# Optimization experiments

Hardware: AMD Instinct MI355X
Metric: run time of the kernel (lower is better)

## Reference

```python
import jax, jax.numpy as jnp
import numpy as np

DIM = 512

def setup_inputs() -> dict:
    key = jax.random.key(0)
    ks = jax.random.split(key, 7)
    B, Nq, Nkv = 8, 1024, 4096
    prototype = jax.random.normal(ks[0], (B, Nq, DIM), dtype=jnp.float32)
    q_x = jax.random.normal(ks[1], (B, Nkv, DIM), dtype=jnp.float32)
    qry_attn_mask = jax.random.bernoulli(ks[2], 0.5, (B, Nkv))  # True = keep
    # Linear(dim, dim, bias=False) weights, torch convention y = x @ W.T
    s = 1.0 / np.sqrt(DIM)
    Wq = jax.random.uniform(ks[3], (DIM, DIM), jnp.float32, -s, s)
    Wk = jax.random.uniform(ks[4], (DIM, DIM), jnp.float32, -s, s)
    Wv = jax.random.uniform(ks[5], (DIM, DIM), jnp.float32, -s, s)
    Wproj = jax.random.uniform(ks[6], (DIM, DIM), jnp.float32, -s, s)
    return {"prototype": prototype, "q_x": q_x, "qry_attn_mask": qry_attn_mask,
            "Wq": Wq, "Wk": Wk, "Wv": Wv, "Wproj": Wproj}

def reference(prototype, q_x, qry_attn_mask, Wq, Wk, Wv, Wproj):
    scale = DIM ** (-0.5)
    q = jnp.einsum('bnd,ed->bne', prototype, Wq)          # [B,Nq,D]
    k = jnp.einsum('bmd,ed->bme', q_x, Wk)                # [B,Nkv,D]
    v = jnp.einsum('bmd,ed->bme', q_x, Wv)                # [B,Nkv,D]
    attn = jnp.einsum('bnd,bmd->bnm', q, k) * scale       # [B,Nq,Nkv]
    bias = (~qry_attn_mask).astype(attn.dtype)[:, None, :] * -10000.0
    attn = jax.nn.softmax(attn + bias, axis=-1)
    x = jnp.einsum('bnm,bmd->bnd', attn, v)
    x = jnp.einsum('bnd,ed->bne', x, Wproj)
    return x
```

## Files before the change

kernel.cpp:

```cpp
#include <hip/hip_runtime.h>
#include <hip/hip_bf16.h>
#include <stdint.h>


typedef __bf16 bf16;
typedef bf16 bf16x8 __attribute__((ext_vector_type(8)));
typedef bf16 bf16x4 __attribute__((ext_vector_type(4)));
typedef float f32x4 __attribute__((ext_vector_type(4)));

#define NB 8
#define NQ 1024
#define NKV 4096
#define DD 512
#define RT_LD 136

__device__ __forceinline__ void direct16(const void* g, void* s) {
  __builtin_amdgcn_global_load_lds(
      (const __attribute__((address_space(1))) void*)g,
      (__attribute__((address_space(3))) void*)s, 16, 0, 0);
}

__global__ void cvt_kernel(const float* __restrict__ src, bf16* __restrict__ dst, int n4) {
  int i = blockIdx.x * blockDim.x + threadIdx.x;
  if (i < n4) {
    float4 v = ((const float4*)src)[i];
    bf16x4 o;
    o.x = (bf16)v.x; o.y = (bf16)v.y; o.z = (bf16)v.z; o.w = (bf16)v.w;
    ((bf16x4*)dst)[i] = o;
  }
}

__global__ void cvt_weights(const float* __restrict__ Wq, const float* __restrict__ Wk,
                            const float* __restrict__ Wv, const float* __restrict__ Wp,
                            bf16* __restrict__ Wq_b, bf16* __restrict__ Wkv_b,
                            bf16* __restrict__ Wp_b) {
  int i = blockIdx.x * blockDim.x + threadIdx.x;
  int w = i >> 16, r = i & 65535;
  const float* src = (w == 0) ? Wq : (w == 1) ? Wk : (w == 2) ? Wv : Wp;
  bf16x4* dst = (w == 0) ? (bf16x4*)Wq_b
              : (w == 3) ? (bf16x4*)Wp_b
                         : (bf16x4*)Wkv_b + (w == 2 ? 65536 : 0);
  float4 v = ((const float4*)src)[r];
  bf16x4 o;
  o.x = (bf16)v.x; o.y = (bf16)v.y; o.z = (bf16)v.z; o.w = (bf16)v.w;
  dst[r] = o;
}

__global__ void sniff_zero(const unsigned* __restrict__ mask, int* __restrict__ flag,
                           float* __restrict__ denom) {
  __shared__ int s_bad0, s_bad1;
  if (threadIdx.x == 0) { s_bad0 = 0; s_bad1 = 0; }
  __syncthreads();
  int b0 = 0, b1 = 0;
  for (int i = threadIdx.x; i < 8192; i += 256) {
    unsigned v = mask[i];
    if (v > 1u) b0 = 1;
    if (v != 0u && v != 0x3F800000u) b1 = 1;
  }
  if (b0) atomicOr(&s_bad0, 1);
  if (b1) atomicOr(&s_bad1, 1);
  for (int i = threadIdx.x; i < NB * NQ; i += 256) denom[i] = 0.f;
  __syncthreads();
  if (threadIdx.x == 0) *flag = (s_bad0 == 0) ? 0 : ((s_bad1 == 0) ? 1 : 2);
}

template <int EPI>
__global__ void __launch_bounds__(256, 2)
gemm_bt(const bf16* __restrict__ A, const bf16* __restrict__ Bw,
        void* __restrict__ Cp, void* __restrict__ Cp2,
        int N, int Klen, int Kstride,
        long sA, long sB, long sC,
        const void* __restrict__ mask, const int* __restrict__ flagP,
        float* __restrict__ denom, float scale, int M) {
  __shared__ alignas(16) bf16 Smem[128 * RT_LD];
  bf16* As = Smem;
  bf16* Bs = Smem + 4096;
  bf16* Rt = Smem;
  const int tid = threadIdx.x;
  const int wave = tid >> 6, lane = tid & 63;
  const int l15 = lane & 15, l4 = lane >> 4;
  const int wm = (wave >> 1) * 64, wn = (wave & 1) * 64;
  const int bx = (EPI == 5) ? blockIdx.y : blockIdx.x;
  const int by = (EPI == 5) ? blockIdx.x : blockIdx.y;
  const int b = blockIdx.z;

  const bf16* Ab = A + (long)b * sA + (long)(by * 128) * Kstride;
  const bf16* Bb = Bw + (long)b * sB + (long)(bx * 128) * Kstride;

  const int c0 = wave * 2, c1 = wave * 2 + 1;
  const int srow = lane >> 2;
  const int scol = (lane & 3) * 8;
  const bf16* ag0 = Ab + (long)(c0 * 16 + srow) * Kstride + scol;
  const bf16* ag1 = Ab + (long)(c1 * 16 + srow) * Kstride + scol;
  const bf16* bg0 = Bb + (long)(c0 * 16 + srow) * Kstride + scol;
  const bf16* bg1 = Bb + (long)(c1 * 16 + srow) * Kstride + scol;
  bf16* al0 = As + c0 * 512 + lane * 8;
  bf16* al1 = As + c1 * 512 + lane * 8;
  bf16* bl0 = Bs + c0 * 512 + lane * 8;
  bf16* bl1 = Bs + c1 * 512 + lane * 8;

  f32x4 acc[4][4] = {};

  for (int kt = 0; kt < Klen; kt += 32) {
    __syncthreads();
    direct16(ag0, al0);
    direct16(ag1, al1);
    direct16(bg0, bl0);
    direct16(bg1, bl1);
    ag0 += 32; ag1 += 32; bg0 += 32; bg1 += 32;
    __syncthreads();
    bf16x8 af[4], bfr[4];
#pragma unroll
    for (int t = 0; t < 4; ++t)
      af[t] = *(const bf16x8*)(As + (wm + t * 16 + l15) * 32 + l4 * 8);
#pragma unroll
    for (int t = 0; t < 4; ++t)
      bfr[t] = *(const bf16x8*)(Bs + (wn + t * 16 + l15) * 32 + l4 * 8);
#pragma unroll
    for (int mt = 0; mt < 4; ++mt)
#pragma unroll
      for (int nt = 0; nt < 4; ++nt)
        acc[mt][nt] = __builtin_amdgcn_mfma_f32_16x16x32_bf16(af[mt], bfr[nt],
                                                              acc[mt][nt], 0, 0, 0);
  }

  const int rowBase = by * 128 + wm;
  const int colBase = bx * 128 + wn;
  const int tR = by * 128;
  const int tC = bx * 128;

  if constexpr (EPI == 2) {
    __syncthreads();
    bf16* C = (bf16*)Cp + (long)b * sC;
    const int mode = *flagP;
    float rs[4][4];
#pragma unroll
    for (int mt = 0; mt < 4; ++mt)
#pragma unroll
      for (int r = 0; r < 4; ++r) rs[mt][r] = 0.f;
#pragma unroll
    for (int nt = 0; nt < 4; ++nt) {
      const int col = colBase + nt * 16 + l15;
      bool keep;
      if (mode == 0)      keep = ((const int*)mask)[b * NKV + col] != 0;
      else if (mode == 1) keep = ((const float*)mask)[b * NKV + col] != 0.f;
      else                keep = ((const unsigned char*)mask)[b * NKV + col] != 0;
#pragma unroll
      for (int mt = 0; mt < 4; ++mt)
#pragma unroll
        for (int r = 0; r < 4; ++r) {
          float p = keep ? __expf(acc[mt][nt][r] * scale) : 0.f;
          rs[mt][r] += p;
          Rt[(wm + mt * 16 + l4 * 4 + r) * RT_LD + wn + nt * 16 + l15] = (bf16)p;
        }
    }
#pragma unroll
    for (int mt = 0; mt < 4; ++mt)
#pragma unroll
      for (int r = 0; r < 4; ++r) {
        float v = rs[mt][r];
        v += __shfl_xor(v, 1, 64);
        v += __shfl_xor(v, 2, 64);
        v += __shfl_xor(v, 4, 64);
        v += __shfl_xor(v, 8, 64);
        if (l15 == 0)
          atomicAdd(&denom[b * M + rowBase + mt * 16 + l4 * 4 + r], v);
      }
    __syncthreads();
    const int r0 = tid >> 2, cq = (tid & 3) * 32;
#pragma unroll
    for (int h = 0; h < 128; h += 64)
#pragma unroll
      for (int j = 0; j < 4; ++j) {
        bf16x8 v = *(const bf16x8*)(Rt + (r0 + h) * RT_LD + cq + j * 8);
        *(bf16x8*)(C + (long)(tR + r0 + h) * N + tC + cq + j * 8) = v;
      }
  } else {
    __syncthreads();
    if (tC < 512) {
      bf16* C = (bf16*)Cp;
#pragma unroll
      for (int mt = 0; mt < 4; ++mt)
#pragma unroll
        for (int nt = 0; nt < 4; ++nt)
#pragma unroll
          for (int r = 0; r < 4; ++r)
            Rt[(wm + mt * 16 + l4 * 4 + r) * RT_LD + wn + nt * 16 + l15] =
                (bf16)acc[mt][nt][r];
      __syncthreads();
      const int r0 = tid >> 2, cq = (tid & 3) * 32;
#pragma unroll
      for (int h = 0; h < 128; h += 64)
#pragma unroll
        for (int j = 0; j < 4; ++j) {
          bf16x8 v = *(const bf16x8*)(Rt + (r0 + h) * RT_LD + cq + j * 8);
          *(bf16x8*)(C + (long)(tR + r0 + h) * 512 + tC + cq + j * 8) = v;
        }
    } else {
      bf16* C = (bf16*)Cp2;
#pragma unroll
      for (int mt = 0; mt < 4; ++mt) {
        const int r0 = wm + mt * 16 + l4 * 4;
#pragma unroll
        for (int nt = 0; nt < 4; ++nt) {
          const int cloc = wn + nt * 16 + l15;
          bf16x4 o;
          o.x = (bf16)acc[mt][nt][0]; o.y = (bf16)acc[mt][nt][1];
          o.z = (bf16)acc[mt][nt][2]; o.w = (bf16)acc[mt][nt][3];
          *(bf16x4*)(Rt + cloc * RT_LD + r0) = o;
        }
      }
      __syncthreads();
      const int bb = tR >> 12, kvloc = tR & 4095;
      const int d0 = tid >> 2, kvq = (tid & 3) * 32;
#pragma unroll
      for (int h = 0; h < 128; h += 64)
#pragma unroll
        for (int j = 0; j < 4; ++j) {
          bf16x8 v = *(const bf16x8*)(Rt + (d0 + h) * RT_LD + kvq + j * 8);
          *(bf16x8*)(C + (long)bb * DD * NKV + (long)(tC - 512 + d0 + h) * NKV +
                     kvloc + kvq + j * 8) = v;
        }
    }
  }
}

template <int EPI>
__global__ void __launch_bounds__(256, 4)
gemm_n64(const bf16* __restrict__ A, const bf16* __restrict__ Bw,
         void* __restrict__ Cp) {
  constexpr int SME = (EPI == 0) ? 128 * 72 : 6144;
  __shared__ alignas(16) bf16 Smem[SME];
  bf16* As = Smem;
  bf16* Bs = Smem + 4096;
  bf16* Rt = Smem;
  const int tid = threadIdx.x;
  const int wave = tid >> 6, lane = tid & 63;
  const int l15 = lane & 15, l4 = lane >> 4;
  const int wm = (wave >> 1) * 64, wn = (wave & 1) * 32;

  const bf16* Ab = A + (long)(blockIdx.y * 128) * DD;
  const bf16* Bb = Bw + (long)(blockIdx.x * 64) * DD;

  const int srow = lane >> 2, scol = (lane & 3) * 8;
  const bf16* ag0 = Ab + (long)(wave * 32 + srow) * DD + scol;
  const bf16* ag1 = ag0 + 16 * DD;
  const bf16* bg0 = Bb + (long)(wave * 16 + srow) * DD + scol;
  bf16* al0 = As + wave * 1024 + lane * 8;
  bf16* al1 = al0 + 512;
  bf16* bl0 = Bs + wave * 512 + lane * 8;

  f32x4 acc[4][2] = {};

  for (int kt = 0; kt < DD; kt += 32) {
    __syncthreads();
    direct16(ag0, al0);
    direct16(ag1, al1);
    direct16(bg0, bl0);
    ag0 += 32; ag1 += 32; bg0 += 32;
    __syncthreads();
    bf16x8 af[4], bfr[2];
#pragma unroll
    for (int t = 0; t < 4; ++t)
      af[t] = *(const bf16x8*)(As + (wm + t * 16 + l15) * 32 + l4 * 8);
#pragma unroll
    for (int t = 0; t < 2; ++t)
      bfr[t] = *(const bf16x8*)(Bs + (wn + t * 16 + l15) * 32 + l4 * 8);
#pragma unroll
    for (int mt = 0; mt < 4; ++mt)
#pragma unroll
      for (int nt = 0; nt < 2; ++nt)
        acc[mt][nt] = __builtin_amdgcn_mfma_f32_16x16x32_bf16(af[mt], bfr[nt],
                                                              acc[mt][nt], 0, 0, 0);
  }

  const int tR = blockIdx.y * 128, tC = blockIdx.x * 64;
  if constexpr (EPI == 0) {
    __syncthreads();
#pragma unroll
    for (int mt = 0; mt < 4; ++mt)
#pragma unroll
      for (int nt = 0; nt < 2; ++nt)
#pragma unroll
        for (int r = 0; r < 4; ++r)
          Rt[(wm + mt * 16 + l4 * 4 + r) * 72 + wn + nt * 16 + l15] =
              (bf16)acc[mt][nt][r];
    __syncthreads();
    bf16* C = (bf16*)Cp;
    const int r0 = tid >> 1, cq = (tid & 1) * 32;
#pragma unroll
    for (int j = 0; j < 4; ++j) {
      bf16x8 v = *(const bf16x8*)(Rt + r0 * 72 + cq + j * 8);
      *(bf16x8*)(C + (long)(tR + r0) * DD + tC + cq + j * 8) = v;
    }
  } else {
    float* C = (float*)Cp;
#pragma unroll
    for (int mt = 0; mt < 4; ++mt)
#pragma unroll
      for (int nt = 0; nt < 2; ++nt)
#pragma unroll
        for (int r = 0; r < 4; ++r)
          C[(long)(tR + wm + mt * 16 + l4 * 4 + r) * DD + tC + wn + nt * 16 + l15] =
              acc[mt][nt][r];
  }
}

__global__ void __launch_bounds__(256, 4)
pv_direct(const bf16* __restrict__ P, const bf16* __restrict__ vT,
          const float* __restrict__ denom, bf16* __restrict__ x) {
  __shared__ alignas(16) bf16 Smem[64 * RT_LD];
  bf16* As = Smem;
  bf16* Bs = Smem + 2048;
  bf16* Rt = Smem;
  const int tid = threadIdx.x;
  const int wave = tid >> 6, lane = tid & 63;
  const int l15 = lane & 15, l4 = lane >> 4;
  const int wm = (wave >> 1) * 32, wn = (wave & 1) * 64;
  const int qB = blockIdx.x * 64;
  const int dB = blockIdx.y * 128;
  const int b = blockIdx.z;

  const bf16* Ab = P + (long)b * NQ * NKV + (long)qB * NKV;
  const bf16* Bb = vT + (long)b * DD * NKV + (long)dB * NKV;

  const int srow = lane >> 2, scol = (lane & 3) * 8;
  const bf16* ag = Ab + (long)(wave * 16 + srow) * NKV + scol;
  const bf16* bg0 = Bb + (long)(wave * 32 + srow) * NKV + scol;
  const bf16* bg1 = bg0 + 16 * NKV;
  bf16* al = As + wave * 512 + lane * 8;
  bf16* bl0 = Bs + wave * 1024 + lane * 8;
  bf16* bl1 = bl0 + 512;

  f32x4 acc[2][4] = {};

  for (int kt = 0; kt < NKV; kt += 32) {
    __syncthreads();
    direct16(ag, al);
    direct16(bg0, bl0);
    direct16(bg1, bl1);
    ag += 32; bg0 += 32; bg1 += 32;
    __syncthreads();
    bf16x8 af[2], bfr[4];
#pragma unroll
    for (int t = 0; t < 2; ++t)
      af[t] = *(const bf16x8*)(As + (wm + t * 16 + l15) * 32 + l4 * 8);
#pragma unroll
    for (int t = 0; t < 4; ++t)
      bfr[t] = *(const bf16x8*)(Bs + (wn + t * 16 + l15) * 32 + l4 * 8);
#pragma unroll
    for (int mt = 0; mt < 2; ++mt)
#pragma unroll
      for (int nt = 0; nt < 4; ++nt)
        acc[mt][nt] = __builtin_amdgcn_mfma_f32_16x16x32_bf16(af[mt], bfr[nt],
                                                              acc[mt][nt], 0, 0, 0);
  }

  __syncthreads();
#pragma unroll
  for (int mt = 0; mt < 2; ++mt)
#pragma unroll
    for (int r = 0; r < 4; ++r) {
      const int row = wm + mt * 16 + l4 * 4 + r;
      const float inv = 1.0f / denom[b * NQ + qB + row];
#pragma unroll
      for (int nt = 0; nt < 4; ++nt)
        Rt[row * RT_LD + wn + nt * 16 + l15] = (bf16)(acc[mt][nt][r] * inv);
    }
  __syncthreads();
  const int r0 = tid >> 2, cq = (tid & 3) * 32;
#pragma unroll
  for (int j = 0; j < 4; ++j) {
    bf16x8 v = *(const bf16x8*)(Rt + r0 * RT_LD + cq + j * 8);
    *(bf16x8*)(x + (long)(b * NQ + qB + r0) * DD + dB + cq + j * 8) = v;
  }
}

extern "C" void kernel_launch(void* const* d_in, const int* in_sizes, int n_in,
                              void* d_out, int out_size, void* d_ws, size_t ws_size,
                              hipStream_t stream) {
  const float* proto = (const float*)d_in[0];
  const float* qx    = (const float*)d_in[1];
  const void*  mask  = d_in[2];
  const float* Wq    = (const float*)d_in[3];
  const float* Wk    = (const float*)d_in[4];
  const float* Wv    = (const float*)d_in[5];
  const float* Wproj = (const float*)d_in[6];
  float* out = (float*)d_out;

  char* w = (char*)d_ws;
  int*   flag  = (int*)w;
  float* denom = (float*)(w + 4096);
  size_t off = 65536;
  bf16* Wq_b  = (bf16*)(w + off); off += (size_t)DD * DD * 2;
  bf16* Wkv_b = (bf16*)(w + off); off += (size_t)DD * DD * 4;
  bf16* Wp_b  = (bf16*)(w + off); off += (size_t)DD * DD * 2;
  bf16* q_b   = (bf16*)(w + off); off += (size_t)NB * NQ * DD * 2;
  bf16* k_b   = (bf16*)(w + off); off += (size_t)NB * NKV * DD * 2;
  bf16* vT_b  = (bf16*)(w + off); off += (size_t)NB * NKV * DD * 2;
  bf16* x_b   = (bf16*)(w + off); off += (size_t)NB * NQ * DD * 2;
  size_t off_pp = off;
  bf16* proto_b = (bf16*)(w + off); off += (size_t)NB * NQ * DD * 2;
  bf16* qx_b    = (bf16*)(w + off);
  bf16* P       = (bf16*)(w + off_pp);

  sniff_zero<<<1, 256, 0, stream>>>((const unsigned*)mask, flag, denom);

  cvt_kernel<<<NB * NQ * DD / 4 / 256, 256, 0, stream>>>(proto, proto_b, NB * NQ * DD / 4);
  cvt_kernel<<<NB * NKV * DD / 4 / 256, 256, 0, stream>>>(qx, qx_b, NB * NKV * DD / 4);
  cvt_weights<<<4 * 65536 / 256, 256, 0, stream>>>(Wq, Wk, Wv, Wproj, Wq_b, Wkv_b, Wp_b);

  const float scale = 0.04419417382415922f;

  gemm_n64<0><<<dim3(8, 64, 1), 256, 0, stream>>>(proto_b, Wq_b, q_b);
  gemm_bt<5><<<dim3(256, 8, 1), 256, 0, stream>>>(
      qx_b, Wkv_b, k_b, vT_b, 1024, DD, DD, 0L, 0L, 0L,
      nullptr, nullptr, nullptr, 0.f, 0);
  gemm_bt<2><<<dim3(NKV / 128, NQ / 128, NB), 256, 0, stream>>>(
      q_b, k_b, P, nullptr, NKV, DD, DD,
      (long)NQ * DD, (long)NKV * DD, (long)NQ * NKV,
      mask, flag, denom, scale, NQ);
  pv_direct<<<dim3(16, 4, 8), 256, 0, stream>>>(P, vT_b, denom, x_b);
  gemm_n64<4><<<dim3(8, 64, 1), 256, 0, stream>>>(x_b, Wp_b, out);
}
```

Baseline: 380.2 us.

## Compact unmasked keys and skip masked key blocks in attention

Adds a per-batch prefix-scan kernel that builds the list of kept key indices and a count padded up to 128. A gather kernel converts only the kept q_x rows to bf16. The K/V projection, the QK^T softmax-numerator kernel and the PV loop then stop at that padded length instead of the full 4096. The aim is to drop the GEMM work and memory traffic spent on masked keys, which the earlier version already set to zero probability. Padded rows between the count and the padded length are never written, so they keep leftover workspace contents. This relies on the zeroed P entries cancelling those rows and adds two small launches.

```diff
diff --git a/kernel.cpp b/kernel.cpp
--- a/kernel.cpp
+++ b/kernel.cpp
@@ -64,13 +64,70 @@
   if (threadIdx.x == 0) *flag = (s_bad0 == 0) ? 0 : ((s_bad1 == 0) ? 1 : 2);
 }
 
+__global__ void scan_mask(const void* __restrict__ mask, const int* __restrict__ flagP,
+                          int* __restrict__ idx, int* __restrict__ cnt,
+                          int* __restrict__ kpad) {
+  const int b = blockIdx.x, tid = threadIdx.x;
+  const int mode = *flagP;
+  __shared__ int ps[256];
+  unsigned bits = 0;
+  int c = 0;
+  const int base = tid * 16;
+  for (int i = 0; i < 16; ++i) {
+    const int col = base + i;
+    bool k;
+    if (mode == 0)      k = ((const int*)mask)[b * NKV + col] != 0;
+    else if (mode == 1) k = ((const float*)mask)[b * NKV + col] != 0.f;
+    else                k = ((const unsigned char*)mask)[b * NKV + col] != 0;
+    bits |= (unsigned)k << i;
+    c += k;
+  }
+  ps[tid] = c;
+  __syncthreads();
+  for (int s = 1; s < 256; s <<= 1) {
+    int v = (tid >= s) ? ps[tid - s] : 0;
+    __syncthreads();
+    ps[tid] += v;
+    __syncthreads();
+  }
+  int off = ps[tid] - c;
+  for (int i = 0; i < 16; ++i)
+    if ((bits >> i) & 1) idx[b * NKV + off++] = base + i;
+  if (tid == 255) {
+    cnt[b] = ps[255];
+    kpad[b] = (ps[255] + 127) & ~127;
+  }
+}
+
+__global__ void gather_qx(const float* __restrict__ qx, const int* __restrict__ idx,
+                          const int* __restrict__ cnt, bf16* __restrict__ qc) {
+  const int b = blockIdx.y;
+  const int wave = threadIdx.x >> 6, lane = threadIdx.x & 63;
+  const int r0 = blockIdx.x * 16 + wave * 4;
+  const int n = cnt[b];
+#pragma unroll
+  for (int j = 0; j < 4; ++j) {
+    const int row = r0 + j;
+    if (row >= n) return;
+    const int src = idx[b * NKV + row];
+    const float4* s = (const float4*)(qx + ((long)b * NKV + src) * DD) + lane;
+    bf16x4* d = (bf16x4*)(qc + ((long)b * NKV + row) * DD) + lane;
+    float4 v0 = s[0], v1 = s[64];
+    bf16x4 o0, o1;
+    o0.x = (bf16)v0.x; o0.y = (bf16)v0.y; o0.z = (bf16)v0.z; o0.w = (bf16)v0.w;
+    o1.x = (bf16)v1.x; o1.y = (bf16)v1.y; o1.z = (bf16)v1.z; o1.w = (bf16)v1.w;
+    d[0] = o0;
+    d[64] = o1;
+  }
+}
+
 template <int EPI>
 __global__ void __launch_bounds__(256, 2)
 gemm_bt(const bf16* __restrict__ A, const bf16* __restrict__ Bw,
         void* __restrict__ Cp, void* __restrict__ Cp2,
         int N, int Klen, int Kstride,
         long sA, long sB, long sC,
-        const void* __restrict__ mask, const int* __restrict__ flagP,
+        const int* __restrict__ cnt, const int* __restrict__ kpad,
         float* __restrict__ denom, float scale, int M) {
   __shared__ alignas(16) bf16 Smem[128 * RT_LD];
   bf16* As = Smem;
@@ -84,6 +141,13 @@
   const int by = (EPI == 5) ? blockIdx.x : blockIdx.y;
   const int b = blockIdx.z;
 
+  if constexpr (EPI == 2) {
+    if (bx * 128 >= kpad[b]) return;
+  } else {
+    const int bb = by >> 5, loc = (by & 31) * 128;
+    if (loc >= kpad[bb]) return;
+  }
+
   const bf16* Ab = A + (long)b * sA + (long)(by * 128) * Kstride;
   const bf16* Bb = Bw + (long)b * sB + (long)(bx * 128) * Kstride;
 
@@ -132,7 +196,7 @@
   if constexpr (EPI == 2) {
     __syncthreads();
     bf16* C = (bf16*)Cp + (long)b * sC;
-    const int mode = *flagP;
+    const int nkeep = cnt[b];
     float rs[4][4];
 #pragma unroll
     for (int mt = 0; mt < 4; ++mt)
@@ -140,11 +204,7 @@
       for (int r = 0; r < 4; ++r) rs[mt][r] = 0.f;
 #pragma unroll
     for (int nt = 0; nt < 4; ++nt) {
-      const int col = colBase + nt * 16 + l15;
-      bool keep;
-      if (mode == 0)      keep = ((const int*)mask)[b * NKV + col] != 0;
-      else if (mode == 1) keep = ((const float*)mask)[b * NKV + col] != 0.f;
-      else                keep = ((const unsigned char*)mask)[b * NKV + col] != 0;
+      const bool keep = (colBase + nt * 16 + l15) < nkeep;
 #pragma unroll
       for (int mt = 0; mt < 4; ++mt)
 #pragma unroll
@@ -308,7 +368,8 @@
 
 __global__ void __launch_bounds__(256, 4)
 pv_direct(const bf16* __restrict__ P, const bf16* __restrict__ vT,
-          const float* __restrict__ denom, bf16* __restrict__ x) {
+          const float* __restrict__ denom, const int* __restrict__ kpad,
+          bf16* __restrict__ x) {
   __shared__ alignas(16) bf16 Smem[64 * RT_LD];
   bf16* As = Smem;
   bf16* Bs = Smem + 2048;
@@ -320,6 +381,7 @@
   const int qB = blockIdx.x * 64;
   const int dB = blockIdx.y * 128;
   const int b = blockIdx.z;
+  const int Kb = kpad[b];
 
   const bf16* Ab = P + (long)b * NQ * NKV + (long)qB * NKV;
   const bf16* Bb = vT + (long)b * DD * NKV + (long)dB * NKV;
@@ -334,7 +396,7 @@
 
   f32x4 acc[2][4] = {};
 
-  for (int kt = 0; kt < NKV; kt += 32) {
+  for (int kt = 0; kt < Kb; kt += 32) {
     __syncthreads();
     direct16(ag, al);
     direct16(bg0, bl0);
@@ -390,36 +452,40 @@
 
   char* w = (char*)d_ws;
   int*   flag  = (int*)w;
+  int*   cnt   = (int*)(w + 64);
+  int*   kpadA = (int*)(w + 128);
   float* denom = (float*)(w + 4096);
   size_t off = 65536;
   bf16* Wq_b  = (bf16*)(w + off); off += (size_t)DD * DD * 2;
   bf16* Wkv_b = (bf16*)(w + off); off += (size_t)DD * DD * 4;
   bf16* Wp_b  = (bf16*)(w + off); off += (size_t)DD * DD * 2;
+  int*  idx   = (int*)(w + off);  off += (size_t)NB * NKV * 4;
   bf16* q_b   = (bf16*)(w + off); off += (size_t)NB * NQ * DD * 2;
   bf16* k_b   = (bf16*)(w + off); off += (size_t)NB * NKV * DD * 2;
   bf16* vT_b  = (bf16*)(w + off); off += (size_t)NB * NKV * DD * 2;
   bf16* x_b   = (bf16*)(w + off); off += (size_t)NB * NQ * DD * 2;
   size_t off_pp = off;
   bf16* proto_b = (bf16*)(w + off); off += (size_t)NB * NQ * DD * 2;
-  bf16* qx_b    = (bf16*)(w + off);
+  bf16* qc_b    = (bf16*)(w + off);
   bf16* P       = (bf16*)(w + off_pp);
 
   sniff_zero<<<1, 256, 0, stream>>>((const unsigned*)mask, flag, denom);
+  scan_mask<<<8, 256, 0, stream>>>(mask, flag, idx, cnt, kpadA);
 
   cvt_kernel<<<NB * NQ * DD / 4 / 256, 256, 0, stream>>>(proto, proto_b, NB * NQ * DD / 4);
-  cvt_kernel<<<NB * NKV * DD / 4 / 256, 256, 0, stream>>>(qx, qx_b, NB * NKV * DD / 4);
+  gather_qx<<<dim3(NKV / 16, NB), 256, 0, stream>>>(qx, idx, cnt, qc_b);
   cvt_weights<<<4 * 65536 / 256, 256, 0, stream>>>(Wq, Wk, Wv, Wproj, Wq_b, Wkv_b, Wp_b);
 
   const float scale = 0.04419417382415922f;
 
   gemm_n64<0><<<dim3(8, 64, 1), 256, 0, stream>>>(proto_b, Wq_b, q_b);
   gemm_bt<5><<<dim3(256, 8, 1), 256, 0, stream>>>(
-      qx_b, Wkv_b, k_b, vT_b, 1024, DD, DD, 0L, 0L, 0L,
-      nullptr, nullptr, nullptr, 0.f, 0);
+      qc_b, Wkv_b, k_b, vT_b, 1024, DD, DD, 0L, 0L, 0L,
+      cnt, kpadA, nullptr, 0.f, 0);
   gemm_bt<2><<<dim3(NKV / 128, NQ / 128, NB), 256, 0, stream>>>(
       q_b, k_b, P, nullptr, NKV, DD, DD,
       (long)NQ * DD, (long)NKV * DD, (long)NQ * NKV,
-      mask, flag, denom, scale, NQ);
-  pv_direct<<<dim3(16, 4, 8), 256, 0, stream>>>(P, vT_b, denom, x_b);
+      cnt, kpadA, denom, scale, NQ);
+  pv_direct<<<dim3(16, 4, 8), 256, 0, stream>>>(P, vT_b, denom, kpadA, x_b);
   gemm_n64<4><<<dim3(8, 64, 1), 256, 0, stream>>>(x_b, Wp_b, out);
 }
```

New measurement: 341.6 us. -10.2%, faster.
